# Kernel tuning notes

Hardware: AMD Instinct MI355X
Metric: run time of the kernel (lower is better)

The kernel has to match this reference:

```python
import jax, jax.numpy as jnp
import numpy as np

NC = 10        # output capsule classes
R = 2048       # num_routes (input capsules)
IN_DIM = 8
OUT_DIM = 16
ITERS = 3
EPS = 1e-8


def squash(s):
    # norm / (1 + norm^2 + eps) * s, over last dim
    norm = jnp.linalg.norm(s, axis=-1, keepdims=True)
    return norm / (1.0 + norm ** 2 + EPS) * s


def setup_inputs() -> dict:
    key = jax.random.key(0)
    k1, k2 = jax.random.split(key)
    x = jax.random.normal(k1, (256, R, IN_DIM), dtype=jnp.float32)
    # W ~ N(0,1) per reset_params
    W = jax.random.normal(k2, (R, IN_DIM, NC * OUT_DIM), dtype=jnp.float32)
    # routing logits b initialized to zeros
    b = jnp.zeros((R, NC), dtype=jnp.float32)
    return {"x": x, "W": W, "b": b}


def reference(x, W, b):
    B = x.shape[0]
    # u_hat: [B, R, NC, OUT_DIM] = x[b,r,:] @ W[r,:,:]
    u_hat = jnp.einsum('bri,rio->bro', x, W).reshape(B, R, NC, OUT_DIM)
    # initial coupling from learned logits b (softmax over classes)
    c = jax.nn.softmax(b, axis=-1)                      # [R, NC]
    s = jnp.sum(c[None, :, :, None] * u_hat, axis=1)    # [B, NC, OUT_DIM]
    v = squash(s)
    # dynamic routing
    bB = jnp.broadcast_to(b, (B, R, NC))
    for _ in range(ITERS):
        # agreement: dot(u_hat, v) over OUT_DIM
        bB = bB + jnp.sum(u_hat * v[:, None, :, :], axis=-1)   # [B, R, NC]
        c = jax.nn.softmax(bB, axis=-1)                          # [B, R, NC]
        s = jnp.sum(c[..., None] * u_hat, axis=1)                # [B, NC, OUT_DIM]
        v = squash(s)
    return v, c
```

## Files before the change

### kernel.cpp

```cpp
#include <hip/hip_runtime.h>
#include <hip/hip_fp16.h>
#include <cstdint>
#include <cstddef>


#define R_   2048
#define NC_  10

typedef _Float16 half8 __attribute__((ext_vector_type(8)));
typedef float   floatx4 __attribute__((ext_vector_type(4)));

__device__ __forceinline__ float rsum16(float x){
  x += __shfl_xor(x, 1, 16);
  x += __shfl_xor(x, 2, 16);
  x += __shfl_xor(x, 4, 16);
  x += __shfl_xor(x, 8, 16);
  return x;
}
__device__ __forceinline__ float sel4(float a, float b, float c, float d, int q){
  float x = (q & 1) ? b : a;
  float y = (q & 1) ? d : c;
  return (q & 2) ? y : x;
}

__global__ __launch_bounds__(256) void pack_x_kernel(const float* __restrict__ x,
                                                     _Float16* __restrict__ xh){
  const int r = blockIdx.x, b = threadIdx.x;
  const float4* xp = (const float4*)(x + ((size_t)b * R_ + r) * 8);
  float4 a = xp[0], c = xp[1];
  half8 h;
  h[0]=(_Float16)a.x; h[1]=(_Float16)a.y; h[2]=(_Float16)a.z; h[3]=(_Float16)a.w;
  h[4]=(_Float16)c.x; h[5]=(_Float16)c.y; h[6]=(_Float16)c.z; h[7]=(_Float16)c.w;
  *(half8*)(xh + ((size_t)r * 256 + b) * 8) = h;
}

__global__ __launch_bounds__(256) void pack_w_kernel(const float* __restrict__ W,
                                                     _Float16* __restrict__ wh){
  const int idx = blockIdx.x * 256 + threadIdx.x;
  const int r = idx / 160, no = idx - r * 160;
  half8 h;
  #pragma unroll
  for (int i = 0; i < 8; ++i) h[i] = (_Float16)W[((size_t)r * 8 + i) * 160 + no];
  *(half8*)(wh + (size_t)idx * 8) = h;
}

__global__ __launch_bounds__(256) void c0_kernel(const float* __restrict__ b_in,
                                                 float* __restrict__ c0){
  int r = blockIdx.x * 256 + threadIdx.x;
  if (r >= R_) return;
  float t[NC_];
  float m = -1e30f;
  #pragma unroll
  for (int n = 0; n < NC_; ++n){ t[n] = b_in[r * NC_ + n]; m = fmaxf(m, t[n]); }
  float sum = 0.f;
  #pragma unroll
  for (int n = 0; n < NC_; ++n){ t[n] = __expf(t[n] - m); sum += t[n]; }
  float inv = 1.f / sum;
  #pragma unroll
  for (int n = 0; n < NC_; ++n) c0[r * NC_ + n] = t[n] * inv;
}

template<int MODE>
__global__ __launch_bounds__(256) void pass_kernel(
    const _Float16* __restrict__ xh,
    const _Float16* __restrict__ wh,
    const float*    __restrict__ c0,
    const float*    __restrict__ b_in,
    float*          __restrict__ bBt,
    float*          __restrict__ c_out,
    const float*    __restrict__ v,
    float*          __restrict__ P)
{
  const int bt  = blockIdx.x >> 6;
  const int rcb = blockIdx.x & 63;
  const int wv  = threadIdx.x >> 6;
  const int lane = threadIdx.x & 63;
  const int q   = lane >> 4;
  const int col = lane & 15;
  const int b0  = bt * 16;
  const int b   = b0 + col;

  float vv[40];
  if (MODE != 0){
    #pragma unroll
    for (int n = 0; n < 10; ++n){
      float4 t4 = *(const float4*)(v + b * 160 + n * 16 + q * 4);
      vv[4*n] = t4.x; vv[4*n+1] = t4.y; vv[4*n+2] = t4.z; vv[4*n+3] = t4.w;
    }
  }
  float acc[40];
  #pragma unroll
  for (int k = 0; k < 40; ++k) acc[k] = 0.f;

  const half8 hz = {0,0,0,0,0,0,0,0};
  const int r0 = rcb * 32 + wv * 8;

  for (int rr = 0; rr < 8; ++rr){
    const int r = r0 + rr;
    half8 bf = hz;
    half8 af[10];
    #pragma unroll
    for (int n = 0; n < 10; ++n) af[n] = hz;
    if (q == 0){
      bf = *(const half8*)(xh + ((size_t)r * 256 + b) * 8);
      #pragma unroll
      for (int n = 0; n < 10; ++n)
        af[n] = *(const half8*)(wh + ((size_t)r * 160 + n * 16 + col) * 8);
    }
    floatx4 C[10];
    #pragma unroll
    for (int n = 0; n < 10; ++n){
      floatx4 z = {0.f, 0.f, 0.f, 0.f};
      C[n] = __builtin_amdgcn_mfma_f32_16x16x32_f16(af[n], bf, z, 0, 0, 0);
    }

    float cc[10];
    if (MODE == 0){
      #pragma unroll
      for (int n = 0; n < 10; ++n) cc[n] = c0[r * 10 + n];
    } else {
      float bn[10];
      #pragma unroll
      for (int n = 0; n < 10; ++n){
        float p =            C[n][0] * vv[4*n];
        p = fmaf(C[n][1], vv[4*n+1], p);
        p = fmaf(C[n][2], vv[4*n+2], p);
        p = fmaf(C[n][3], vv[4*n+3], p);
        p += __shfl_xor(p, 16, 64);
        p += __shfl_xor(p, 32, 64);
        float bold = (MODE == 1) ? b_in[r * 10 + n]
                                 : bBt[((size_t)r * 10 + n) * 256 + b];
        bn[n] = bold + p;
      }
      float m = bn[0];
      #pragma unroll
      for (int n = 1; n < 10; ++n) m = fmaxf(m, bn[n]);
      float sum = 0.f;
      #pragma unroll
      for (int n = 0; n < 10; ++n){ cc[n] = __expf(bn[n] - m); sum += cc[n]; }
      float inv = 1.f / sum;
      #pragma unroll
      for (int n = 0; n < 10; ++n) cc[n] *= inv;

      if (MODE == 3){
        const size_t base = ((size_t)b * R_ + r) * 10;
        c_out[base + q]     = sel4(cc[0], cc[1], cc[2], cc[3], q);
        c_out[base + q + 4] = sel4(cc[4], cc[5], cc[6], cc[7], q);
        if (q < 2) c_out[base + q + 8] = (q & 1) ? cc[9] : cc[8];
      } else {
        bBt[((size_t)r * 10 + q)     * 256 + b] = sel4(bn[0], bn[1], bn[2], bn[3], q);
        bBt[((size_t)r * 10 + q + 4) * 256 + b] = sel4(bn[4], bn[5], bn[6], bn[7], q);
        if (q < 2) bBt[((size_t)r * 10 + q + 8) * 256 + b] = (q & 1) ? bn[9] : bn[8];
      }
    }
    #pragma unroll
    for (int n = 0; n < 10; ++n){
      acc[4*n]   = fmaf(cc[n], C[n][0], acc[4*n]);
      acc[4*n+1] = fmaf(cc[n], C[n][1], acc[4*n+1]);
      acc[4*n+2] = fmaf(cc[n], C[n][2], acc[4*n+2]);
      acc[4*n+3] = fmaf(cc[n], C[n][3], acc[4*n+3]);
    }
  }

  __shared__ float red[4 * 2560];
  const int off = col * 160 + q * 4;
  #pragma unroll
  for (int n = 0; n < 10; ++n){
    #pragma unroll
    for (int j = 0; j < 4; ++j)
      red[wv * 2560 + off + n * 16 + j] = acc[4*n + j];
  }
  __syncthreads();
  float* Pd = P + ((size_t)rcb * 256 + b0) * 160;
  for (int k = threadIdx.x; k < 2560; k += 256)
    Pd[k] = (red[k] + red[2560 + k]) + (red[5120 + k] + red[7680 + k]);
}

template<bool FINAL>
__global__ __launch_bounds__(256) void reduce_squash(const float* __restrict__ P,
                                                     float* __restrict__ vout){
  int g = blockIdx.x * 256 + threadIdx.x;
  float s0 = 0.f, s1 = 0.f;
  #pragma unroll 8
  for (int j = 0; j < 64; j += 2){
    s0 += P[(size_t)j * 40960 + g];
    s1 += P[(size_t)(j + 1) * 40960 + g];
  }
  float s = s0 + s1;
  float ss = rsum16(s * s);
  float f = sqrtf(ss) / (1.f + ss + 1e-8f);
  vout[g] = f * s;
}

extern "C" void kernel_launch(void* const* d_in, const int* in_sizes, int n_in,
                              void* d_out, int out_size, void* d_ws, size_t ws_size,
                              hipStream_t stream){
  const float* x    = (const float*)d_in[0];
  const float* W    = (const float*)d_in[1];
  const float* b_in = (const float*)d_in[2];
  float* out   = (float*)d_out;
  float* out_v = out;
  float* c_out = out + 40960;

  char* w = (char*)d_ws;
  _Float16* xh = (_Float16*)w;
  _Float16* wh = (_Float16*)(w + 8388608);
  float* bBt   = (float*)(w + 13631488);
  float* P     = (float*)(w + 34603008);
  float* v     = (float*)(w + 45088768);
  float* c0    = (float*)(w + 45252608);

  pack_x_kernel<<<R_, 256, 0, stream>>>(x, xh);
  pack_w_kernel<<<1280, 256, 0, stream>>>(W, wh);
  c0_kernel<<<8, 256, 0, stream>>>(b_in, c0);

  pass_kernel<0><<<1024, 256, 0, stream>>>(xh, wh, c0, b_in, bBt, c_out, v, P);
  reduce_squash<false><<<160, 256, 0, stream>>>(P, v);
  pass_kernel<1><<<1024, 256, 0, stream>>>(xh, wh, c0, b_in, bBt, c_out, v, P);
  reduce_squash<false><<<160, 256, 0, stream>>>(P, v);
  pass_kernel<2><<<1024, 256, 0, stream>>>(xh, wh, c0, b_in, bBt, c_out, v, P);
  reduce_squash<false><<<160, 256, 0, stream>>>(P, v);
  pass_kernel<3><<<1024, 256, 0, stream>>>(xh, wh, c0, b_in, bBt, c_out, v, P);
  reduce_squash<true><<<160, 256, 0, stream>>>(P, out_v);
}
```

Baseline: 280.3 us.

## Recompute MFMA products instead of holding them to cut register pressure

The pass kernel no longer keeps all ten 16x16 MFMA results live across the softmax. It issues the MFMAs twice, once for the agreement logits and once for the weighted accumulation, and reloads W fragments each time. Launch bounds now request 3 blocks per SM. The LDS reduction drops one wave's buffer, pads rows to avoid bank conflicts, and has wave 0 add its own registers and write float4 results. This trades duplicated MFMA work and W loads for lower register use and higher occupancy.

```diff
diff --git a/kernel.cpp b/kernel.cpp
--- a/kernel.cpp
+++ b/kernel.cpp
@@ -61,7 +61,7 @@
 }
 
 template<int MODE>
-__global__ __launch_bounds__(256) void pass_kernel(
+__global__ __launch_bounds__(256, 3) void pass_kernel(
     const _Float16* __restrict__ xh,
     const _Float16* __restrict__ wh,
     const float*    __restrict__ c0,
@@ -93,87 +93,91 @@
   for (int k = 0; k < 40; ++k) acc[k] = 0.f;
 
   const half8 hz = {0,0,0,0,0,0,0,0};
+  const floatx4 z4 = {0.f, 0.f, 0.f, 0.f};
   const int r0 = rcb * 32 + wv * 8;
 
   for (int rr = 0; rr < 8; ++rr){
     const int r = r0 + rr;
     half8 bf = hz;
-    half8 af[10];
-    #pragma unroll
-    for (int n = 0; n < 10; ++n) af[n] = hz;
-    if (q == 0){
-      bf = *(const half8*)(xh + ((size_t)r * 256 + b) * 8);
-      #pragma unroll
-      for (int n = 0; n < 10; ++n)
-        af[n] = *(const half8*)(wh + ((size_t)r * 160 + n * 16 + col) * 8);
-    }
-    floatx4 C[10];
-    #pragma unroll
-    for (int n = 0; n < 10; ++n){
-      floatx4 z = {0.f, 0.f, 0.f, 0.f};
-      C[n] = __builtin_amdgcn_mfma_f32_16x16x32_f16(af[n], bf, z, 0, 0, 0);
-    }
+    if (q == 0) bf = *(const half8*)(xh + ((size_t)r * 256 + b) * 8);
 
     float cc[10];
     if (MODE == 0){
       #pragma unroll
       for (int n = 0; n < 10; ++n) cc[n] = c0[r * 10 + n];
     } else {
-      float bn[10];
       #pragma unroll
       for (int n = 0; n < 10; ++n){
-        float p =            C[n][0] * vv[4*n];
-        p = fmaf(C[n][1], vv[4*n+1], p);
-        p = fmaf(C[n][2], vv[4*n+2], p);
-        p = fmaf(C[n][3], vv[4*n+3], p);
+        half8 af = hz;
+        if (q == 0) af = *(const half8*)(wh + ((size_t)r * 160 + n * 16 + col) * 8);
+        floatx4 C = __builtin_amdgcn_mfma_f32_16x16x32_f16(af, bf, z4, 0, 0, 0);
+        float p = C[0] * vv[4*n];
+        p = fmaf(C[1], vv[4*n+1], p);
+        p = fmaf(C[2], vv[4*n+2], p);
+        p = fmaf(C[3], vv[4*n+3], p);
         p += __shfl_xor(p, 16, 64);
         p += __shfl_xor(p, 32, 64);
         float bold = (MODE == 1) ? b_in[r * 10 + n]
                                  : bBt[((size_t)r * 10 + n) * 256 + b];
-        bn[n] = bold + p;
+        cc[n] = bold + p;
       }
-      float m = bn[0];
-      #pragma unroll
-      for (int n = 1; n < 10; ++n) m = fmaxf(m, bn[n]);
+      if (MODE != 3){
+        bBt[((size_t)r * 10 + q)     * 256 + b] = sel4(cc[0], cc[1], cc[2], cc[3], q);
+        bBt[((size_t)r * 10 + q + 4) * 256 + b] = sel4(cc[4], cc[5], cc[6], cc[7], q);
+        if (q < 2) bBt[((size_t)r * 10 + q + 8) * 256 + b] = (q & 1) ? cc[9] : cc[8];
+      }
+      float m = cc[0];
+      #pragma unroll
+      for (int n = 1; n < 10; ++n) m = fmaxf(m, cc[n]);
       float sum = 0.f;
       #pragma unroll
-      for (int n = 0; n < 10; ++n){ cc[n] = __expf(bn[n] - m); sum += cc[n]; }
+      for (int n = 0; n < 10; ++n){ cc[n] = __expf(cc[n] - m); sum += cc[n]; }
       float inv = 1.f / sum;
       #pragma unroll
       for (int n = 0; n < 10; ++n) cc[n] *= inv;
-
       if (MODE == 3){
         const size_t base = ((size_t)b * R_ + r) * 10;
         c_out[base + q]     = sel4(cc[0], cc[1], cc[2], cc[3], q);
         c_out[base + q + 4] = sel4(cc[4], cc[5], cc[6], cc[7], q);
         if (q < 2) c_out[base + q + 8] = (q & 1) ? cc[9] : cc[8];
-      } else {
-        bBt[((size_t)r * 10 + q)     * 256 + b] = sel4(bn[0], bn[1], bn[2], bn[3], q);
-        bBt[((size_t)r * 10 + q + 4) * 256 + b] = sel4(bn[4], bn[5], bn[6], bn[7], q);
-        if (q < 2) bBt[((size_t)r * 10 + q + 8) * 256 + b] = (q & 1) ? bn[9] : bn[8];
       }
     }
-    #pragma unroll
-    for (int n = 0; n < 10; ++n){
-      acc[4*n]   = fmaf(cc[n], C[n][0], acc[4*n]);
-      acc[4*n+1] = fmaf(cc[n], C[n][1], acc[4*n+1]);
-      acc[4*n+2] = fmaf(cc[n], C[n][2], acc[4*n+2]);
-      acc[4*n+3] = fmaf(cc[n], C[n][3], acc[4*n+3]);
-    }
-  }
-
-  __shared__ float red[4 * 2560];
-  const int off = col * 160 + q * 4;
-  #pragma unroll
-  for (int n = 0; n < 10; ++n){
-    #pragma unroll
-    for (int j = 0; j < 4; ++j)
-      red[wv * 2560 + off + n * 16 + j] = acc[4*n + j];
+
+    #pragma unroll
+    for (int n = 0; n < 10; ++n){
+      half8 af = hz;
+      if (q == 0) af = *(const half8*)(wh + ((size_t)r * 160 + n * 16 + col) * 8);
+      floatx4 C = __builtin_amdgcn_mfma_f32_16x16x32_f16(af, bf, z4, 0, 0, 0);
+      acc[4*n]   = fmaf(cc[n], C[0], acc[4*n]);
+      acc[4*n+1] = fmaf(cc[n], C[1], acc[4*n+1]);
+      acc[4*n+2] = fmaf(cc[n], C[2], acc[4*n+2]);
+      acc[4*n+3] = fmaf(cc[n], C[3], acc[4*n+3]);
+    }
+  }
+
+  __shared__ float red[3 * 2624];
+  if (wv > 0){
+    float* rp = red + (wv - 1) * 2624 + col * 164 + q * 4;
+    #pragma unroll
+    for (int n = 0; n < 10; ++n){
+      rp[n*16+0] = acc[4*n];   rp[n*16+1] = acc[4*n+1];
+      rp[n*16+2] = acc[4*n+2]; rp[n*16+3] = acc[4*n+3];
+    }
   }
   __syncthreads();
-  float* Pd = P + ((size_t)rcb * 256 + b0) * 160;
-  for (int k = threadIdx.x; k < 2560; k += 256)
-    Pd[k] = (red[k] + red[2560 + k]) + (red[5120 + k] + red[7680 + k]);
+  if (wv == 0){
+    const float* rp = red + col * 164 + q * 4;
+    float* Pd = P + (((size_t)rcb * 256) + b) * 160 + q * 4;
+    #pragma unroll
+    for (int n = 0; n < 10; ++n){
+      float4 o;
+      o.x = acc[4*n]   + rp[n*16]   + rp[2624 + n*16]   + rp[5248 + n*16];
+      o.y = acc[4*n+1] + rp[n*16+1] + rp[2624 + n*16+1] + rp[5248 + n*16+1];
+      o.z = acc[4*n+2] + rp[n*16+2] + rp[2624 + n*16+2] + rp[5248 + n*16+2];
+      o.w = acc[4*n+3] + rp[n*16+3] + rp[2624 + n*16+3] + rp[5248 + n*16+3];
+      *(float4*)(Pd + n * 16) = o;
+    }
+  }
 }
 
 template<bool FINAL>
```

After: 542.4 us. +93.5%, slower.
